# Kernel optimization log

Measured on AMD Instinct MI355X. Metric: run time of the kernel, lower is better.

Reference implementation:

```python
import jax, jax.numpy as jnp
import numpy as np

B, N, CIN, COUT, R, K = 8, 4096, 64, 128, 32, 3
GROUPS = 8
GN_EPS = 1e-5


def setup_inputs() -> dict:
    key = jax.random.key(0)
    ks = jax.random.split(key, 6)
    w = lambda k, shape, fan: jax.random.normal(k, shape, jnp.float32) / np.sqrt(fan)
    return dict(
        features=jax.random.normal(ks[0], (B, CIN, N), jnp.float32),
        coords=jax.random.uniform(ks[1], (B, N, 3), jnp.float32),
        conv1_w=w(ks[2], (COUT, CIN, K, K, K), CIN * K ** 3), conv1_b=jnp.zeros((COUT,), jnp.float32),
        gn1_g=jnp.ones((COUT,), jnp.float32), gn1_b=jnp.zeros((COUT,), jnp.float32),
        conv2_w=w(ks[3], (COUT, COUT, K, K, K), COUT * K ** 3), conv2_b=jnp.zeros((COUT,), jnp.float32),
        gn2_g=jnp.ones((COUT,), jnp.float32), gn2_b=jnp.zeros((COUT,), jnp.float32),
        pt_w=w(ks[4], (COUT, CIN), CIN), pt_b=jnp.zeros((COUT,), jnp.float32),
        ptgn_g=jnp.ones((COUT,), jnp.float32), ptgn_b=jnp.zeros((COUT,), jnp.float32),
    )


def swish(x):
    return x * jax.nn.sigmoid(x)


def group_norm(x, gamma, beta):
    # x: [B, C, *spatial]
    b, c = x.shape[0], x.shape[1]
    sp = x.shape[2:]
    xg = x.reshape(b, GROUPS, -1)
    m = xg.mean(-1, keepdims=True)
    v = xg.var(-1, keepdims=True)
    xg = (xg - m) * jax.lax.rsqrt(v + GN_EPS)
    x = xg.reshape(b, c, *sp)
    shape = (1, c) + (1,) * len(sp)
    return x * gamma.reshape(shape) + beta.reshape(shape)


def conv3d(x, w, bias):
    p = K // 2
    y = jax.lax.conv_general_dilated(
        x, w, window_strides=(1, 1, 1), padding=[(p, p)] * 3,
        dimension_numbers=('NCDHW', 'OIDHW', 'NCDHW'))
    return y + bias[None, :, None, None, None]


def voxelize(features, coords):
    # PVCNN avg_voxelize: normalize coords to [0, R-1], round, scatter-mean.
    c = coords - coords.mean(axis=1, keepdims=True)          # [B,N,3]
    scale = 2.0 * jnp.linalg.norm(c, axis=-1).max(axis=1)     # [B], eps=0
    norm_coords = c / scale[:, None, None] + 0.5
    norm_coords = jnp.clip(norm_coords * R, 0.0, R - 1)       # float coords in [0, R-1]
    vox = jnp.round(norm_coords).astype(jnp.int32)
    flat = (vox[..., 0] * R + vox[..., 1]) * R + vox[..., 2]  # [B,N]
    seg = (flat + jnp.arange(B, dtype=jnp.int32)[:, None] * R ** 3).reshape(-1)
    ft = features.transpose(0, 2, 1).reshape(B * N, CIN)
    sums = jax.ops.segment_sum(ft, seg, num_segments=B * R ** 3)
    cnt = jax.ops.segment_sum(jnp.ones((B * N,), ft.dtype), seg, num_segments=B * R ** 3)
    grid = sums / jnp.maximum(cnt, 1.0)[:, None]
    grid = grid.reshape(B, R ** 3, CIN).transpose(0, 2, 1).reshape(B, CIN, R, R, R)
    return grid, norm_coords


def trilinear_devoxelize(grid, norm_coords):
    # grid: [B, C, R, R, R]; norm_coords: [B, N, 3] float in [0, R-1]
    c = grid.shape[1]
    f = jnp.floor(norm_coords)
    d = norm_coords - f                                       # frac, [B,N,3]
    f0 = f.astype(jnp.int32)
    f1 = jnp.minimum(f0 + 1, R - 1)
    gridf = grid.reshape(B, c, R ** 3)
    out = jnp.zeros((B, c, N), grid.dtype)
    for ix in (0, 1):
        for iy in (0, 1):
            for iz in (0, 1):
                xi = f1[..., 0] if ix else f0[..., 0]
                yi = f1[..., 1] if iy else f0[..., 1]
                zi = f1[..., 2] if iz else f0[..., 2]
                wx = d[..., 0] if ix else 1.0 - d[..., 0]
                wy = d[..., 1] if iy else 1.0 - d[..., 1]
                wz = d[..., 2] if iz else 1.0 - d[..., 2]
                idx = (xi * R + yi) * R + zi                  # [B,N]
                g = jnp.take_along_axis(gridf, idx[:, None, :], axis=2)  # [B,C,N]
                out = out + g * (wx * wy * wz)[:, None, :]
    return out


def reference(features, coords, conv1_w, conv1_b, gn1_g, gn1_b,
              conv2_w, conv2_b, gn2_g, gn2_b, pt_w, pt_b, ptgn_g, ptgn_b):
    grid, norm_coords = voxelize(features, coords)
    h = swish(group_norm(conv3d(grid, conv1_w, conv1_b), gn1_g, gn1_b))
    h = swish(group_norm(conv3d(h, conv2_w, conv2_b), gn2_g, gn2_b))
    devox = trilinear_devoxelize(h, norm_coords)              # [B, COUT, N]
    pf = jnp.einsum('oc,bcn->bon', pt_w, features) + pt_b[None, :, None]
    pf = swish(group_norm(pf, ptgn_g, ptgn_b))
    return devox + pf
```

## Files before the change

### kernel.cpp

```cpp
#include <hip/hip_runtime.h>
#include <hip/hip_bf16.h>
#include <cstdint>

#define B_ 8
#define N_ 4096
#define CIN_ 64
#define COUT_ 128
#define R_ 32
#define R3_ 32768
#define GROUPS_ 8
#define EPS_ 1e-5f

typedef float f32x4 __attribute__((ext_vector_type(4)));
typedef __bf16 bf16x8 __attribute__((ext_vector_type(8)));
typedef unsigned short ushort8x __attribute__((ext_vector_type(8)));

static __device__ __forceinline__ unsigned short f2b(float f) {
    uint32_t u = __float_as_uint(f);
    uint32_t r = (u + 0x7fffu + ((u >> 16) & 1u)) >> 16;
    return (unsigned short)r;
}
static __device__ __forceinline__ float b2f(unsigned short u) {
    return __uint_as_float(((uint32_t)u) << 16);
}
static __device__ __forceinline__ float fswish(float s) {
    return s * __builtin_amdgcn_rcpf(1.0f + __expf(-s));
}

__global__ void k_batch_stats(const float* __restrict__ coords, float* __restrict__ bstats) {
    int b = blockIdx.x;
    int tid = threadIdx.x;
    __shared__ float rb[256];
    __shared__ float smean[3];
    const float* cb = coords + (size_t)b * N_ * 3;
    float sx = 0.f, sy = 0.f, sz = 0.f;
    for (int n = tid; n < N_; n += 256) {
        sx += cb[n * 3 + 0];
        sy += cb[n * 3 + 1];
        sz += cb[n * 3 + 2];
    }
    float vals[3] = {sx, sy, sz};
    for (int k = 0; k < 3; ++k) {
        rb[tid] = vals[k];
        __syncthreads();
        for (int s = 128; s > 0; s >>= 1) {
            if (tid < s) rb[tid] += rb[tid + s];
            __syncthreads();
        }
        if (tid == 0) smean[k] = rb[0] / (float)N_;
        __syncthreads();
    }
    float mx = smean[0], my = smean[1], mz = smean[2];
    float m2 = 0.f;
    for (int n = tid; n < N_; n += 256) {
        float dx = cb[n * 3 + 0] - mx, dy = cb[n * 3 + 1] - my, dz = cb[n * 3 + 2] - mz;
        m2 = fmaxf(m2, dx * dx + dy * dy + dz * dz);
    }
    rb[tid] = m2;
    __syncthreads();
    for (int s = 128; s > 0; s >>= 1) {
        if (tid < s) rb[tid] = fmaxf(rb[tid], rb[tid + s]);
        __syncthreads();
    }
    if (tid == 0) {
        bstats[b * 4 + 0] = mx;
        bstats[b * 4 + 1] = my;
        bstats[b * 4 + 2] = mz;
        bstats[b * 4 + 3] = 2.0f * sqrtf(rb[0]);
    }
}

__global__ void k_points(const float* __restrict__ coords, const float* __restrict__ bstats,
                         float* __restrict__ ncoords, int* __restrict__ flatidx,
                         float* __restrict__ cnt) {
    int idx = blockIdx.x * 256 + threadIdx.x;
    int b = idx >> 12, n = idx & (N_ - 1);
    float scale = bstats[b * 4 + 3];
    int vi[3];
    for (int k = 0; k < 3; ++k) {
        float c = coords[((size_t)b * N_ + n) * 3 + k] - bstats[b * 4 + k];
        float nc = fminf(fmaxf((c / scale + 0.5f) * (float)R_, 0.0f), (float)(R_ - 1));
        ncoords[((size_t)b * N_ + n) * 3 + k] = nc;
        vi[k] = (int)rintf(nc);
    }
    int flat = (vi[0] * R_ + vi[1]) * R_ + vi[2];
    flatidx[idx] = flat;
    atomicAdd(&cnt[(size_t)b * R3_ + flat], 1.0f);
}

__global__ void k_scatter(const float* __restrict__ feat, const int* __restrict__ flatidx,
                          float* __restrict__ vox, int b0) {
    int bid = blockIdx.x;
    int nch = bid & 15, ci = (bid >> 4) & 63, bl = bid >> 10;
    int b = b0 + bl;
    int n = nch * 256 + threadIdx.x;
    float v = feat[((size_t)b * CIN_ + ci) * N_ + n];
    int flat = flatidx[b * N_ + n];
    atomicAdd(&vox[((size_t)bl * R3_ + flat) * CIN_ + ci], v);
}

__global__ void k_divide(const float* __restrict__ vox, const float* __restrict__ cnt,
                         unsigned short* __restrict__ gA, int b0) {
    size_t idx8 = (size_t)blockIdx.x * 256 + threadIdx.x;
    size_t voxel = idx8 >> 3;
    float c = cnt[(size_t)b0 * R3_ + voxel];
    float s = 1.0f / fmaxf(c, 1.0f);
    const float4* v4 = (const float4*)vox;
    float4 a = v4[idx8 * 2], b = v4[idx8 * 2 + 1];
    ushort8x o;
    o[0] = f2b(a.x * s); o[1] = f2b(a.y * s); o[2] = f2b(a.z * s); o[3] = f2b(a.w * s);
    o[4] = f2b(b.x * s); o[5] = f2b(b.y * s); o[6] = f2b(b.z * s); o[7] = f2b(b.w * s);
    ((ushort8x*)gA)[idx8] = o;
}

__global__ void k_feat2b(const float* __restrict__ f, unsigned short* __restrict__ fb, int b0) {
    size_t i8 = (size_t)blockIdx.x * 256 + threadIdx.x;
    const float4* s = (const float4*)(f + (size_t)b0 * CIN_ * N_);
    float4 a = s[i8 * 2], b = s[i8 * 2 + 1];
    ushort8x o;
    o[0] = f2b(a.x); o[1] = f2b(a.y); o[2] = f2b(a.z); o[3] = f2b(a.w);
    o[4] = f2b(b.x); o[5] = f2b(b.y); o[6] = f2b(b.z); o[7] = f2b(b.w);
    ((ushort8x*)fb)[i8] = o;
}

__global__ void k_wpack16(const float* __restrict__ w, unsigned short* __restrict__ wp,
                          int Cin, int taps) {
    int e = blockIdx.x * 256 + threadIdx.x;
    int total = taps * Cin * 128;
    if (e >= total) return;
    int KC = Cin / 32;
    int j = e & 7;
    int l = (e >> 3) & 63;
    int rest = e >> 9;
    int ct = rest & 7;
    int stepk = rest >> 3;
    int kc = stepk % KC;
    int t = stepk / KC;
    int co = ct * 16 + (l & 15);
    int ci = kc * 32 + (l >> 4) * 8 + j;
    wp[e] = f2b(w[((size_t)co * Cin + ci) * taps + t]);
}

template <int CIN, bool FUSEGN>
__global__ __launch_bounds__(256) void k_conv16(
    const unsigned short* __restrict__ in, const unsigned short* __restrict__ wp,
    const float* __restrict__ bias, const float* __restrict__ instats,
    const float* __restrict__ ingamma, const float* __restrict__ inbeta,
    unsigned short* __restrict__ out, float* __restrict__ stats, int b0) {
    constexpr int KC = CIN / 32;
    constexpr int S = CIN + 8;
    __shared__ unsigned short abuf[6 * 34 * S];
    __shared__ float s_sum[8], s_sq[8];
    __shared__ __align__(16) float sA[128], sB[128];
    int tid = threadIdx.x;
    int bid = blockIdx.x;
    int yg = bid & 7, x = (bid >> 3) & 31, bl = bid >> 8;
    int y0 = yg * 4;
    int lane = tid & 63, wv = tid >> 6;
    int yp = wv & 1, zt = wv >> 1;
    int mrow = lane & 15, quad = lane >> 4;

    if (tid < 8) { s_sum[tid] = 0.f; s_sq[tid] = 0.f; }
    if (FUSEGN && tid < 128) {
        int b = b0 + bl;
        int grp = tid >> 4;
        const float ic = 1.0f / (16.0f * R3_);
        float mean = instats[(b * 8 + grp) * 2 + 0] * ic;
        float var = instats[(b * 8 + grp) * 2 + 1] * ic - mean * mean;
        float inv = rsqrtf(var + EPS_);
        float A = ingamma[tid] * inv;
        sA[tid] = A;
        sB[tid] = inbeta[tid] - mean * A;
    }
    for (int i = tid; i < 6 * 2 * (CIN / 8); i += 256) {
        int cy = i / (2 * (CIN / 8));
        int r = i - cy * (2 * (CIN / 8));
        int hz = (r >= (CIN / 8)) ? 33 : 0;
        int c8 = r % (CIN / 8);
        ushort8x zz = {0, 0, 0, 0, 0, 0, 0, 0};
        *(ushort8x*)&abuf[(cy * 34 + hz) * S + c8 * 8] = zz;
    }

    float bv[8];
#pragma unroll
    for (int ct = 0; ct < 8; ++ct) bv[ct] = bias[ct * 16 + mrow];
    f32x4 acc[2][8];
#pragma unroll
    for (int yo2 = 0; yo2 < 2; ++yo2)
#pragma unroll
        for (int ct = 0; ct < 8; ++ct) {
            acc[yo2][ct][0] = bv[ct]; acc[yo2][ct][1] = bv[ct];
            acc[yo2][ct][2] = bv[ct]; acc[yo2][ct][3] = bv[ct];
        }

    for (int xxi = 0; xxi < 3; ++xxi) {
        int xx = x + xxi - 1;
        if (xx < 0 || xx >= 32) continue;
        __syncthreads();
        for (int i = tid; i < 6 * 32 * (CIN / 8); i += 256) {
            int cy = i / (32 * (CIN / 8));
            int r = i - cy * (32 * (CIN / 8));
            int z = r / (CIN / 8), c8 = r - z * (CIN / 8);
            int yy = y0 - 1 + cy;
            ushort8x v = {0, 0, 0, 0, 0, 0, 0, 0};
            if (yy >= 0 && yy < 32) {
                v = *(const ushort8x*)&in[((size_t)bl * R3_ + xx * 1024 + yy * 32 + z) * CIN + c8 * 8];
                if (FUSEGN) {
                    float4 A0 = *(const float4*)&sA[c8 * 8];
                    float4 A1 = *(const float4*)&sA[c8 * 8 + 4];
                    float4 B0 = *(const float4*)&sB[c8 * 8];
                    float4 B1 = *(const float4*)&sB[c8 * 8 + 4];
                    v[0] = f2b(fswish(A0.x * b2f(v[0]) + B0.x));
                    v[1] = f2b(fswish(A0.y * b2f(v[1]) + B0.y));
                    v[2] = f2b(fswish(A0.z * b2f(v[2]) + B0.z));
                    v[3] = f2b(fswish(A0.w * b2f(v[3]) + B0.w));
                    v[4] = f2b(fswish(A1.x * b2f(v[4]) + B1.x));
                    v[5] = f2b(fswish(A1.y * b2f(v[5]) + B1.y));
                    v[6] = f2b(fswish(A1.z * b2f(v[6]) + B1.z));
                    v[7] = f2b(fswish(A1.w * b2f(v[7]) + B1.w));
                }
            }
            *(ushort8x*)&abuf[(cy * 34 + z + 1) * S + c8 * 8] = v;
        }
        __syncthreads();

        for (int dy3 = 0; dy3 < 3; ++dy3) {
            for (int dz = 0; dz < 3; ++dz) {
                int t = (xxi * 3 + dy3) * 3 + dz;
#pragma unroll
                for (int kc = 0; kc < KC; ++kc) {
                    const unsigned short* wbase =
                        wp + ((size_t)((t * KC + kc) * 8) * 64 + lane) * 8;
                    bf16x8 bfr[8];
#pragma unroll
                    for (int ct = 0; ct < 8; ++ct)
                        bfr[ct] = *(const bf16x8*)(wbase + ct * 512);
#pragma unroll
                    for (int yo2 = 0; yo2 < 2; ++yo2) {
                        int cy = yp * 2 + yo2 + dy3;
                        bf16x8 a = *(const bf16x8*)
                            &abuf[(cy * 34 + zt * 16 + mrow + dz) * S + kc * 32 + quad * 8];
#pragma unroll
                        for (int ct = 0; ct < 8; ++ct)
                            acc[yo2][ct] = __builtin_amdgcn_mfma_f32_16x16x32_bf16(
                                a, bfr[ct], acc[yo2][ct], 0, 0, 0);
                    }
                }
            }
        }
    }

    float lsum[8] = {0.f, 0.f, 0.f, 0.f, 0.f, 0.f, 0.f, 0.f};
    float lsq[8] = {0.f, 0.f, 0.f, 0.f, 0.f, 0.f, 0.f, 0.f};
#pragma unroll
    for (int yo2 = 0; yo2 < 2; ++yo2) {
        int y = y0 + yp * 2 + yo2;
        unsigned short* obase = out + ((size_t)bl * R3_ + x * 1024 + y * 32) * 128;
#pragma unroll
        for (int ct = 0; ct < 8; ++ct) {
            int co = ct * 16 + mrow;
#pragma unroll
            for (int r = 0; r < 4; ++r) {
                int z = zt * 16 + quad * 4 + r;
                float vv = acc[yo2][ct][r];
                obase[(size_t)z * 128 + co] = f2b(vv);
                lsum[ct] += vv;
                lsq[ct] += vv * vv;
            }
        }
    }
#pragma unroll
    for (int ct = 0; ct < 8; ++ct) {
        float s = lsum[ct], q = lsq[ct];
#pragma unroll
        for (int off = 32; off >= 1; off >>= 1) {
            s += __shfl_xor(s, off);
            q += __shfl_xor(q, off);
        }
        if (lane == 0) {
            atomicAdd(&s_sum[ct], s);
            atomicAdd(&s_sq[ct], q);
        }
    }
    __syncthreads();
    if (tid < 8) {
        int b = b0 + bl;
        atomicAdd(&stats[((size_t)b * 8 + tid) * 2 + 0], s_sum[tid]);
        atomicAdd(&stats[((size_t)b * 8 + tid) * 2 + 1], s_sq[tid]);
    }
}

__global__ __launch_bounds__(256) void k_point_mfma(
    const unsigned short* __restrict__ featb, const unsigned short* __restrict__ wp,
    const float* __restrict__ bias, unsigned short* __restrict__ pf,
    float* __restrict__ stats, int b0) {
    __shared__ __align__(16) unsigned short ALds[256 * 72];
    int tid = threadIdx.x;
    int bid = blockIdx.x;
    int bl = bid >> 4;
    int n0 = (bid & 15) * 256;
    int b = b0 + bl;
    int lane = tid & 63, wv = tid >> 6;
    int nh = wv & 1, ch = wv >> 1;
    int mrow = lane & 15, quad = lane >> 4;

    {
        int c0 = (tid >> 5) * 8;
        int nl = tid & 31;
        for (int u = 0; u < 8; ++u) {
            int n = u * 32 + nl;
            ushort8x v;
#pragma unroll
            for (int k = 0; k < 8; ++k)
                v[k] = featb[((size_t)(bl * 64 + c0 + k)) * N_ + n0 + n];
            *(ushort8x*)&ALds[n * 72 + c0] = v;
        }
    }

    bf16x8 bfr[2][4];
#pragma unroll
    for (int kc = 0; kc < 2; ++kc)
#pragma unroll
        for (int ct = 0; ct < 4; ++ct)
            bfr[kc][ct] = *(const bf16x8*)&wp[((size_t)((kc * 8) + ch * 4 + ct) * 64 + lane) * 8];

    float bv[4];
#pragma unroll
    for (int ct = 0; ct < 4; ++ct) bv[ct] = bias[ch * 64 + ct * 16 + mrow];
    f32x4 acc[8][4];
#pragma unroll
    for (int mt = 0; mt < 8; ++mt)
#pragma unroll
        for (int ct = 0; ct < 4; ++ct) {
            acc[mt][ct][0] = bv[ct]; acc[mt][ct][1] = bv[ct];
            acc[mt][ct][2] = bv[ct]; acc[mt][ct][3] = bv[ct];
        }

    __syncthreads();
#pragma unroll
    for (int kc = 0; kc < 2; ++kc) {
#pragma unroll
        for (int mt = 0; mt < 8; ++mt) {
            bf16x8 a = *(const bf16x8*)
                &ALds[(nh * 128 + mt * 16 + mrow) * 72 + kc * 32 + quad * 8];
#pragma unroll
            for (int ct = 0; ct < 4; ++ct)
                acc[mt][ct] = __builtin_amdgcn_mfma_f32_16x16x32_bf16(
                    a, bfr[kc][ct], acc[mt][ct], 0, 0, 0);
        }
    }

#pragma unroll
    for (int ct = 0; ct < 4; ++ct) {
        int co = ch * 64 + ct * 16 + mrow;
        float s = 0.f, q = 0.f;
#pragma unroll
        for (int mt = 0; mt < 8; ++mt) {
#pragma unroll
            for (int r = 0; r < 4; ++r) {
                int n = nh * 128 + mt * 16 + quad * 4 + r;
                float vv = acc[mt][ct][r];
                pf[((size_t)bl * N_ + n0 + n) * 128 + co] = f2b(vv);
                s += vv;
                q += vv * vv;
            }
        }
#pragma unroll
        for (int off = 32; off >= 1; off >>= 1) {
            s += __shfl_xor(s, off);
            q += __shfl_xor(q, off);
        }
        if (lane == 0) {
            int g = ch * 4 + ct;
            atomicAdd(&stats[((size_t)b * 8 + g) * 2 + 0], s);
            atomicAdd(&stats[((size_t)b * 8 + g) * 2 + 1], q);
        }
    }
}

__global__ __launch_bounds__(256) void k_final(
    const unsigned short* __restrict__ grid, const float* __restrict__ ncoords,
    const unsigned short* __restrict__ pf,
    const float* __restrict__ stats2, const float* __restrict__ g2g,
    const float* __restrict__ g2b,
    const float* __restrict__ statsPt, const float* __restrict__ pgg,
    const float* __restrict__ pgb,
    float* __restrict__ out, int b0) {
    __shared__ int sidx[32][8];
    __shared__ float swt[32][8];
    __shared__ float devt[32 * 129];
    int bid = blockIdx.x;
    int bl = bid >> 7;
    int b = b0 + bl;
    int n0 = (bid & 127) * 32;
    int tid = threadIdx.x;
    if (tid < 32) {
        int n = n0 + tid;
        const float* nc = ncoords + ((size_t)b * N_ + n) * 3;
        float fc[3] = {nc[0], nc[1], nc[2]};
        int i0[3], i1[3];
        float dd[3];
        for (int k = 0; k < 3; ++k) {
            float fl = floorf(fc[k]);
            i0[k] = (int)fl;
            i1[k] = min(i0[k] + 1, R_ - 1);
            dd[k] = fc[k] - fl;
        }
#pragma unroll
        for (int k = 0; k < 8; ++k) {
            int ix = (k >> 2) & 1, iy = (k >> 1) & 1, iz = k & 1;
            int xi = ix ? i1[0] : i0[0];
            int yi = iy ? i1[1] : i0[1];
            int zi = iz ? i1[2] : i0[2];
            sidx[tid][k] = (xi * R_ + yi) * R_ + zi;
            float wx = ix ? dd[0] : 1.0f - dd[0];
            float wy = iy ? dd[1] : 1.0f - dd[1];
            float wz = iz ? dd[2] : 1.0f - dd[2];
            swt[tid][k] = wx * wy * wz;
        }
    }
    __syncthreads();
    int co = tid & 127, pg = tid >> 7;
    int grp = co >> 4;
    const float ic2 = 1.0f / (16.0f * R3_);
    float mean2 = stats2[(b * 8 + grp) * 2 + 0] * ic2;
    float var2 = stats2[(b * 8 + grp) * 2 + 1] * ic2 - mean2 * mean2;
    float inv2 = rsqrtf(var2 + EPS_);
    float A2 = g2g[co] * inv2, B2 = g2b[co] - mean2 * A2;
    const float icp = 1.0f / (16.0f * N_);
    float meanp = statsPt[(b * 8 + grp) * 2 + 0] * icp;
    float varp = statsPt[(b * 8 + grp) * 2 + 1] * icp - meanp * meanp;
    float invp = rsqrtf(varp + EPS_);
    float Ap = pgg[co] * invp, Bp = pgb[co] - meanp * Ap;

    const unsigned short* gp = grid + (size_t)bl * R3_ * 128 + co;
    for (int p = pg; p < 32; p += 2) {
        float acc = 0.f;
#pragma unroll
        for (int k = 0; k < 8; ++k) {
            float s = A2 * b2f(gp[(size_t)sidx[p][k] * 128]) + B2;
            acc += swt[p][k] * fswish(s);
        }
        float xv = b2f(pf[((size_t)bl * N_ + n0 + p) * 128 + co]);
        devt[p * 129 + co] = acc + fswish(Ap * xv + Bp);
    }
    __syncthreads();
    int pp = tid & 31, cg = tid >> 5;
    float* op = out + (size_t)b * 128 * N_ + n0 + pp;
    for (int c = cg * 16; c < cg * 16 + 16; ++c)
        op[(size_t)c * N_] = devt[pp * 129 + c];
}

extern "C" void kernel_launch(void* const* d_in, const int* in_sizes, int n_in,
                              void* d_out, int out_size, void* d_ws, size_t ws_size,
                              hipStream_t stream) {
    const float* features = (const float*)d_in[0];
    const float* coords = (const float*)d_in[1];
    const float* c1w = (const float*)d_in[2];
    const float* c1b = (const float*)d_in[3];
    const float* g1g = (const float*)d_in[4];
    const float* g1b = (const float*)d_in[5];
    const float* c2w = (const float*)d_in[6];
    const float* c2b = (const float*)d_in[7];
    const float* g2g = (const float*)d_in[8];
    const float* g2b = (const float*)d_in[9];
    const float* ptw = (const float*)d_in[10];
    const float* ptb = (const float*)d_in[11];
    const float* pgg = (const float*)d_in[12];
    const float* pgb = (const float*)d_in[13];
    float* outp = (float*)d_out;

    size_t globals = ((size_t)B_ * R3_ * 4 + 255 & ~(size_t)255)
                   + ((size_t)B_ * N_ * 3 * 4 + 255 & ~(size_t)255)
                   + ((size_t)B_ * N_ * 4 + 255 & ~(size_t)255)
                   + 256 + 2048
                   + ((size_t)27 * 64 * 128 * 2 + 255 & ~(size_t)255)
                   + ((size_t)27 * 128 * 128 * 2 + 255 & ~(size_t)255)
                   + ((size_t)64 * 128 * 2 + 255 & ~(size_t)255)
                   + 8192;
    int CB = 1;
    for (int cb = 8; cb >= 1; cb >>= 1) {
        size_t need = globals
                    + ((size_t)cb * R3_ * 64 * 4)
                    + ((size_t)cb * R3_ * 64 * 2)
                    + ((size_t)cb * R3_ * 128 * 2)
                    + ((size_t)cb * N_ * 128 * 2)
                    + ((size_t)cb * 64 * N_ * 2);
        if (need <= ws_size) { CB = cb; break; }
    }

    char* ws = (char*)d_ws;
    size_t o = 0;
    auto alloc = [&](size_t bytes) {
        size_t r = o;
        o += (bytes + 255) & ~(size_t)255;
        return r;
    };
    float* voxC = (float*)(ws + alloc((size_t)CB * R3_ * 64 * 4));
    unsigned short* gC = (unsigned short*)voxC;
    unsigned short* gA = (unsigned short*)(ws + alloc((size_t)CB * R3_ * 64 * 2));
    unsigned short* gB = (unsigned short*)(ws + alloc((size_t)CB * R3_ * 128 * 2));
    unsigned short* pfbuf = (unsigned short*)(ws + alloc((size_t)CB * N_ * 128 * 2));
    unsigned short* featbc = (unsigned short*)(ws + alloc((size_t)CB * 64 * N_ * 2));
    float* cnt = (float*)(ws + alloc((size_t)B_ * R3_ * 4));
    float* ncoords = (float*)(ws + alloc((size_t)B_ * N_ * 3 * 4));
    int* flatidx = (int*)(ws + alloc((size_t)B_ * N_ * 4));
    float* bstats = (float*)(ws + alloc(256));
    float* statsAll = (float*)(ws + alloc(2048));
    float* stats1 = statsAll;
    float* stats2 = statsAll + 128;
    float* statsPt = statsAll + 256;
    unsigned short* wp1 = (unsigned short*)(ws + alloc((size_t)27 * 64 * 128 * 2));
    unsigned short* wp2 = (unsigned short*)(ws + alloc((size_t)27 * 128 * 128 * 2));
    unsigned short* wpPt = (unsigned short*)(ws + alloc((size_t)64 * 128 * 2));

    hipMemsetAsync(cnt, 0, (size_t)B_ * R3_ * 4, stream);
    hipMemsetAsync(statsAll, 0, 1536, stream);
    k_wpack16<<<(27 * 64 * 128 + 255) / 256, 256, 0, stream>>>(c1w, wp1, 64, 27);
    k_wpack16<<<(27 * 128 * 128 + 255) / 256, 256, 0, stream>>>(c2w, wp2, 128, 27);
    k_wpack16<<<(64 * 128 + 255) / 256, 256, 0, stream>>>(ptw, wpPt, 64, 1);
    k_batch_stats<<<B_, 256, 0, stream>>>(coords, bstats);
    k_points<<<B_ * N_ / 256, 256, 0, stream>>>(coords, bstats, ncoords, flatidx, cnt);

    for (int b0 = 0; b0 < B_; b0 += CB) {
        hipMemsetAsync(voxC, 0, (size_t)CB * R3_ * 64 * 4, stream);
        k_feat2b<<<CB * 128, 256, 0, stream>>>(features, featbc, b0);
        k_scatter<<<CB * 64 * 16, 256, 0, stream>>>(features, flatidx, voxC, b0);
        k_divide<<<CB * 1024, 256, 0, stream>>>(voxC, cnt, gA, b0);
        k_conv16<64, false><<<CB * 256, 256, 0, stream>>>(
            gA, wp1, c1b, nullptr, nullptr, nullptr, gB, stats1, b0);
        k_conv16<128, true><<<CB * 256, 256, 0, stream>>>(
            gB, wp2, c2b, stats1, g1g, g1b, gC, stats2, b0);
        k_point_mfma<<<CB * 16, 256, 0, stream>>>(featbc, wpPt, ptb, pfbuf, statsPt, b0);
        k_final<<<CB * 128, 256, 0, stream>>>(gC, ncoords, pfbuf,
                                              stats2, g2g, g2b, statsPt, pgg, pgb, outp, b0);
    }
}
```

Baseline: 713.3 us.

## Halve conv block waves with 4-row accumulators and split GN-swish into standalone pass

```diff
diff --git a/kernel.cpp b/kernel.cpp
--- a/kernel.cpp
+++ b/kernel.cpp
@@ -141,38 +141,45 @@
     wp[e] = f2b(w[((size_t)co * Cin + ci) * taps + t]);
 }
 
-template <int CIN, bool FUSEGN>
-__global__ __launch_bounds__(256) void k_conv16(
+__global__ void k_gnswish(unsigned short* __restrict__ g, const float* __restrict__ stats,
+                          const float* __restrict__ gamma, const float* __restrict__ beta,
+                          int b0) {
+    size_t idx8 = (size_t)blockIdx.x * 256 + threadIdx.x;
+    int c0 = (int)(idx8 & 15) * 8;
+    int b = b0 + (int)(idx8 >> 19);
+    int grp = c0 >> 4;
+    const float cntv = 16.0f * R3_;
+    float mean = stats[(b * 8 + grp) * 2 + 0] / cntv;
+    float var = stats[(b * 8 + grp) * 2 + 1] / cntv - mean * mean;
+    float inv = rsqrtf(var + EPS_);
+    ushort8x v = ((ushort8x*)g)[idx8];
+#pragma unroll
+    for (int k = 0; k < 8; ++k) {
+        float A = gamma[c0 + k] * inv;
+        float Bc = beta[c0 + k] - mean * A;
+        v[k] = f2b(fswish(A * b2f(v[k]) + Bc));
+    }
+    ((ushort8x*)g)[idx8] = v;
+}
+
+template <int CIN>
+__global__ __launch_bounds__(128, 2) void k_conv16(
     const unsigned short* __restrict__ in, const unsigned short* __restrict__ wp,
-    const float* __restrict__ bias, const float* __restrict__ instats,
-    const float* __restrict__ ingamma, const float* __restrict__ inbeta,
-    unsigned short* __restrict__ out, float* __restrict__ stats, int b0) {
+    const float* __restrict__ bias, unsigned short* __restrict__ out,
+    float* __restrict__ stats, int b0) {
     constexpr int KC = CIN / 32;
     constexpr int S = CIN + 8;
     __shared__ unsigned short abuf[6 * 34 * S];
     __shared__ float s_sum[8], s_sq[8];
-    __shared__ __align__(16) float sA[128], sB[128];
     int tid = threadIdx.x;
     int bid = blockIdx.x;
     int yg = bid & 7, x = (bid >> 3) & 31, bl = bid >> 8;
     int y0 = yg * 4;
-    int lane = tid & 63, wv = tid >> 6;
-    int yp = wv & 1, zt = wv >> 1;
+    int lane = tid & 63, zt = tid >> 6;
     int mrow = lane & 15, quad = lane >> 4;
 
     if (tid < 8) { s_sum[tid] = 0.f; s_sq[tid] = 0.f; }
-    if (FUSEGN && tid < 128) {
-        int b = b0 + bl;
-        int grp = tid >> 4;
-        const float ic = 1.0f / (16.0f * R3_);
-        float mean = instats[(b * 8 + grp) * 2 + 0] * ic;
-        float var = instats[(b * 8 + grp) * 2 + 1] * ic - mean * mean;
-        float inv = rsqrtf(var + EPS_);
-        float A = ingamma[tid] * inv;
-        sA[tid] = A;
-        sB[tid] = inbeta[tid] - mean * A;
-    }
-    for (int i = tid; i < 6 * 2 * (CIN / 8); i += 256) {
+    for (int i = tid; i < 6 * 2 * (CIN / 8); i += 128) {
         int cy = i / (2 * (CIN / 8));
         int r = i - cy * (2 * (CIN / 8));
         int hz = (r >= (CIN / 8)) ? 33 : 0;
@@ -184,42 +191,27 @@
     float bv[8];
 #pragma unroll
     for (int ct = 0; ct < 8; ++ct) bv[ct] = bias[ct * 16 + mrow];
-    f32x4 acc[2][8];
-#pragma unroll
-    for (int yo2 = 0; yo2 < 2; ++yo2)
+    f32x4 acc[4][8];
+#pragma unroll
+    for (int yc = 0; yc < 4; ++yc)
 #pragma unroll
         for (int ct = 0; ct < 8; ++ct) {
-            acc[yo2][ct][0] = bv[ct]; acc[yo2][ct][1] = bv[ct];
-            acc[yo2][ct][2] = bv[ct]; acc[yo2][ct][3] = bv[ct];
+            acc[yc][ct][0] = bv[ct]; acc[yc][ct][1] = bv[ct];
+            acc[yc][ct][2] = bv[ct]; acc[yc][ct][3] = bv[ct];
         }
 
     for (int xxi = 0; xxi < 3; ++xxi) {
         int xx = x + xxi - 1;
         if (xx < 0 || xx >= 32) continue;
         __syncthreads();
-        for (int i = tid; i < 6 * 32 * (CIN / 8); i += 256) {
+        for (int i = tid; i < 6 * 32 * (CIN / 8); i += 128) {
             int cy = i / (32 * (CIN / 8));
             int r = i - cy * (32 * (CIN / 8));
             int z = r / (CIN / 8), c8 = r - z * (CIN / 8);
             int yy = y0 - 1 + cy;
             ushort8x v = {0, 0, 0, 0, 0, 0, 0, 0};
-            if (yy >= 0 && yy < 32) {
+            if (yy >= 0 && yy < 32)
                 v = *(const ushort8x*)&in[((size_t)bl * R3_ + xx * 1024 + yy * 32 + z) * CIN + c8 * 8];
-                if (FUSEGN) {
-                    float4 A0 = *(const float4*)&sA[c8 * 8];
-                    float4 A1 = *(const float4*)&sA[c8 * 8 + 4];
-                    float4 B0 = *(const float4*)&sB[c8 * 8];
-                    float4 B1 = *(const float4*)&sB[c8 * 8 + 4];
-                    v[0] = f2b(fswish(A0.x * b2f(v[0]) + B0.x));
-                    v[1] = f2b(fswish(A0.y * b2f(v[1]) + B0.y));
-                    v[2] = f2b(fswish(A0.z * b2f(v[2]) + B0.z));
-                    v[3] = f2b(fswish(A0.w * b2f(v[3]) + B0.w));
-                    v[4] = f2b(fswish(A1.x * b2f(v[4]) + B1.x));
-                    v[5] = f2b(fswish(A1.y * b2f(v[5]) + B1.y));
-                    v[6] = f2b(fswish(A1.z * b2f(v[6]) + B1.z));
-                    v[7] = f2b(fswish(A1.w * b2f(v[7]) + B1.w));
-                }
-            }
             *(ushort8x*)&abuf[(cy * 34 + z + 1) * S + c8 * 8] = v;
         }
         __syncthreads();
@@ -236,14 +228,14 @@
                     for (int ct = 0; ct < 8; ++ct)
                         bfr[ct] = *(const bf16x8*)(wbase + ct * 512);
 #pragma unroll
-                    for (int yo2 = 0; yo2 < 2; ++yo2) {
-                        int cy = yp * 2 + yo2 + dy3;
+                    for (int yc = 0; yc < 4; ++yc) {
+                        int cy = yc + dy3;
                         bf16x8 a = *(const bf16x8*)
                             &abuf[(cy * 34 + zt * 16 + mrow + dz) * S + kc * 32 + quad * 8];
 #pragma unroll
                         for (int ct = 0; ct < 8; ++ct)
-                            acc[yo2][ct] = __builtin_amdgcn_mfma_f32_16x16x32_bf16(
-                                a, bfr[ct], acc[yo2][ct], 0, 0, 0);
+                            acc[yc][ct] = __builtin_amdgcn_mfma_f32_16x16x32_bf16(
+                                a, bfr[ct], acc[yc][ct], 0, 0, 0);
                     }
                 }
             }
@@ -253,8 +245,8 @@
     float lsum[8] = {0.f, 0.f, 0.f, 0.f, 0.f, 0.f, 0.f, 0.f};
     float lsq[8] = {0.f, 0.f, 0.f, 0.f, 0.f, 0.f, 0.f, 0.f};
 #pragma unroll
-    for (int yo2 = 0; yo2 < 2; ++yo2) {
-        int y = y0 + yp * 2 + yo2;
+    for (int yc = 0; yc < 4; ++yc) {
+        int y = y0 + yc;
         unsigned short* obase = out + ((size_t)bl * R3_ + x * 1024 + y * 32) * 128;
 #pragma unroll
         for (int ct = 0; ct < 8; ++ct) {
@@ -262,7 +254,7 @@
 #pragma unroll
             for (int r = 0; r < 4; ++r) {
                 int z = zt * 16 + quad * 4 + r;
-                float vv = acc[yo2][ct][r];
+                float vv = acc[yc][ct][r];
                 obase[(size_t)z * 128 + co] = f2b(vv);
                 lsum[ct] += vv;
                 lsq[ct] += vv * vv;
@@ -527,10 +519,9 @@
         k_feat2b<<<CB * 128, 256, 0, stream>>>(features, featbc, b0);
         k_scatter<<<CB * 64 * 16, 256, 0, stream>>>(features, flatidx, voxC, b0);
         k_divide<<<CB * 1024, 256, 0, stream>>>(voxC, cnt, gA, b0);
-        k_conv16<64, false><<<CB * 256, 256, 0, stream>>>(
-            gA, wp1, c1b, nullptr, nullptr, nullptr, gB, stats1, b0);
-        k_conv16<128, true><<<CB * 256, 256, 0, stream>>>(
-            gB, wp2, c2b, stats1, g1g, g1b, gC, stats2, b0);
+        k_conv16<64><<<CB * 256, 128, 0, stream>>>(gA, wp1, c1b, gB, stats1, b0);
+        k_gnswish<<<CB * 2048, 256, 0, stream>>>(gB, stats1, g1g, g1b, b0);
+        k_conv16<128><<<CB * 256, 128, 0, stream>>>(gB, wp2, c2b, gC, stats2, b0);
         k_point_mfma<<<CB * 16, 256, 0, stream>>>(featbc, wpPt, ptb, pfbuf, statsPt, b0);
         k_final<<<CB * 128, 256, 0, stream>>>(gC, ncoords, pfbuf,
                                               stats2, g2g, g2b, statsPt, pgg, pgb, outp, b0);
```

Result: slower. 763.1 us (+7.0%).
